# Performance work log

Measured on AMD Instinct MI355X. Metric: run time of the kernel, lower is better.

Reference implementation:

```python
import jax, jax.numpy as jnp
import numpy as np

EPS = 1e-5
L = 19        # number of semantic labels (fc_mu0..fc_mu18)
S = 512       # style_length


def conv3x3(x, w, b):
    # x: [B,C,H,W], w: [O,I,3,3] (torch OIHW), b: [O]
    y = jax.lax.conv_general_dilated(
        x, w, window_strides=(1, 1), padding='SAME',
        dimension_numbers=('NCHW', 'OIHW', 'NCHW'))
    return y + b[None, :, None, None]


def setup_inputs() -> dict:
    key = jax.random.key(0)
    ks = jax.random.split(key, 20)
    B, FIN, H, W = 4, 128, 256, 256
    inp = {
        'x': jax.random.normal(ks[0], (B, FIN, H, W), jnp.float32),
        'labels': jax.random.randint(ks[1], (B, H, W), 0, L),
        'noise': jax.random.normal(ks[2], (B, W, H, 1), jnp.float32),
        'style_codes': jax.random.normal(ks[3], (B, L, S), jnp.float32),
        # params
        'noise_var': 0.02 * jax.random.normal(ks[4], (FIN,), jnp.float32),
        'w_sh': 0.02 * jax.random.normal(ks[5], (128, L, 3, 3), jnp.float32),
        'b_sh': jnp.zeros((128,), jnp.float32),
        'w_g': 0.02 * jax.random.normal(ks[6], (FIN, 128, 3, 3), jnp.float32),
        'b_g': jnp.zeros((FIN,), jnp.float32),
        'w_b': 0.02 * jax.random.normal(ks[7], (FIN, 128, 3, 3), jnp.float32),
        'b_b': jnp.zeros((FIN,), jnp.float32),
        'Wfc': 0.02 * jax.random.normal(ks[8], (L, S, S), jnp.float32),  # [label, out, in]
        'bfc': jnp.zeros((L, S), jnp.float32),
        'w_cg': 0.02 * jax.random.normal(ks[9], (FIN, S, 3, 3), jnp.float32),
        'b_cg': jnp.zeros((FIN,), jnp.float32),
        'w_cb': 0.02 * jax.random.normal(ks[10], (FIN, S, 3, 3), jnp.float32),
        'b_cb': jnp.zeros((FIN,), jnp.float32),
        'g_blend': jnp.zeros((1,), jnp.float32),
        'b_blend': jnp.zeros((1,), jnp.float32),
    }
    return inp


def reference(x, labels, noise, style_codes, noise_var, w_sh, b_sh, w_g, b_g,
              w_b, b_b, Wfc, bfc, w_cg, b_cg, w_cb, b_cb, g_blend, b_blend):
    B, FIN, H, W = x.shape
    # added_noise: randn([B,W,H,1]) * noise_var[FIN] then transpose(1,3) -> [B,FIN,H,W]
    added = jnp.transpose(noise * noise_var, (0, 3, 2, 1))
    xn = x + added
    # param-free BatchNorm2d (training-mode batch stats, biased var)
    mean = jnp.mean(xn, axis=(0, 2, 3), keepdims=True)
    var = jnp.mean(jnp.square(xn - mean), axis=(0, 2, 3), keepdims=True)
    normalized = (xn - mean) / jnp.sqrt(var + EPS)

    # one-hot segmap [B,L,H,W]; interpolation to x's size is identity here
    seg = jnp.transpose(jax.nn.one_hot(labels, L, dtype=x.dtype), (0, 3, 1, 2))

    # per-label style FC: mu[b,j,:] = relu(fc_mu_j(style_codes[b,j]))
    mu = jax.nn.relu(jnp.einsum('bjd,jod->bjo', style_codes, Wfc) + bfc)  # [B,L,S]
    # masked_scatter with one-hot masks == per-pixel gather of the label's style code
    middle = mu[jnp.arange(B)[:, None, None], labels]        # [B,H,W,S]
    middle = jnp.transpose(middle, (0, 3, 1, 2))              # [B,S,H,W]

    gamma_avg = conv3x3(middle, w_cg, b_cg)
    beta_avg = conv3x3(middle, w_cb, b_cb)

    actv = jax.nn.relu(conv3x3(seg, w_sh, b_sh))
    gamma_spade = conv3x3(actv, w_g, b_g)
    beta_spade = conv3x3(actv, w_b, b_b)

    ga = jax.nn.sigmoid(g_blend)
    ba = jax.nn.sigmoid(b_blend)
    gamma_final = ga * gamma_avg + (1.0 - ga) * gamma_spade
    beta_final = ba * beta_avg + (1.0 - ba) * beta_spade
    return normalized * (1.0 + gamma_final) + beta_final
```

## Files before the change

kernel.cpp:

```cpp
#include <hip/hip_runtime.h>
#include <hip/hip_bf16.h>

#define NB   4
#define FIN  128
#define HH   256
#define WWW  256
#define LLAB 19
#define SSTY 512
#define HW   (HH*WWW)
#define NRED (NB*HW)

#define WS_NT   0
#define WS_SUM  262144
#define WS_SSQ  262272
#define WS_MEAN 262400
#define WS_ISTD 262528
#define WS_MU   262656
#define WS_A2   301568
#define WS_S1N  476672
#define WS_S2N  476673
#define WS_BSTG_B 1906752
#define WS_WSH_B  4855872

#define ASTRIDE 5200
#define OHSTRIDE 80

typedef __attribute__((ext_vector_type(8))) short bf16x8;
typedef __attribute__((ext_vector_type(4))) float f32x4;

__device__ inline unsigned short f2bf(float f) {
  __hip_bfloat16 h = __float2bfloat16(f);
  union { __hip_bfloat16 h; unsigned short u; } cv; cv.h = h; return cv.u;
}
__device__ inline float bf2f(short u) {
  union { unsigned int u; float f; } cv;
  cv.u = ((unsigned int)(unsigned short)u) << 16; return cv.f;
}

__device__ inline void gload_lds16(const void* g, void* l) {
  __builtin_amdgcn_global_load_lds(
      (const __attribute__((address_space(1))) void*)g,
      (__attribute__((address_space(3))) void*)l, 16, 0, 0);
}

__global__ __launch_bounds__(256) void kprep1(const float* __restrict__ noise,
                                              const float* __restrict__ style,
                                              const float* __restrict__ Wfc,
                                              const float* __restrict__ bfc,
                                              const float* __restrict__ w_g,
                                              const float* __restrict__ w_b,
                                              const float* __restrict__ w_sh,
                                              const float* __restrict__ g_blend,
                                              const float* __restrict__ b_blend,
                                              const float* __restrict__ x,
                                              char* __restrict__ wsb,
                                              float* __restrict__ ws) {
  const int t = threadIdx.x;
  if (blockIdx.x < 256) {
    __shared__ float tile[32][33];
    int blk = blockIdx.x;
    int b = blk >> 6, by = (blk >> 3) & 7, bx = blk & 7;
    int w0 = bx * 32, h0 = by * 32;
    int txx = t & 31, tyy = t >> 5;
    #pragma unroll
    for (int j = 0; j < 4; ++j) {
      int wi = w0 + tyy + j * 8;
      tile[tyy + j * 8][txx] = noise[(size_t)(b * 256 + wi) * 256 + h0 + txx];
    }
    __syncthreads();
    #pragma unroll
    for (int j = 0; j < 4; ++j) {
      int hi = h0 + tyy + j * 8;
      ws[WS_NT + (size_t)(b * 256 + hi) * 256 + w0 + txx] = tile[txx][tyy + j * 8];
    }
  } else if (blockIdx.x < 408) {
    int m = blockIdx.x - 256;
    int j = m >> 3, r = m & 7, b = r >> 1, half = r & 1;
    int o = half * 256 + t;
    const float4* wrow = (const float4*)(Wfc + ((size_t)j * 512 + o) * 512);
    const float4* srow = (const float4*)(style + ((size_t)b * 19 + j) * 512);
    float acc = 0.f;
    for (int d = 0; d < 128; ++d) {
      float4 w = wrow[d];
      float4 s = srow[d];
      acc = fmaf(w.x, s.x, acc); acc = fmaf(w.y, s.y, acc);
      acc = fmaf(w.z, s.z, acc); acc = fmaf(w.w, s.w, acc);
    }
    acc += bfc[j * 512 + o];
    ws[WS_MU + ((size_t)b * 19 + j) * 512 + o] = fmaxf(acc, 0.f);
  } else if (blockIdx.x < 552) {
    int tid = (blockIdx.x - 408) * 256 + t;
    int lane = tid & 63, grp = tid >> 6;
    int s36 = grp % 36, nb = grp / 36;
    int kk = s36 >> 2, cb = s36 & 3;
    int n = nb * 16 + (lane & 15);
    int conv = n & 1, cout = n >> 1;
    float blend = conv ? b_blend[0] : g_blend[0];
    float scale = 1.f - 1.f / (1.f + __expf(-blend));
    const float* src = conv ? w_b : w_g;
    bf16x8 v;
    #pragma unroll
    for (int i = 0; i < 8; ++i) {
      int k = s36 * 32 + (lane >> 4) * 8 + i;
      int kki = k >> 7, cin = k & 127;
      v[i] = (short)f2bf(scale * src[((size_t)cout * 128 + cin) * 9 + kki]);
    }
    size_t slot = (size_t)(kk * 5 + cb) * 16384 + (size_t)(nb * 64 + lane) * 16;
    #pragma unroll
    for (int bb2 = 0; bb2 < 4; ++bb2)
      *(bf16x8*)(wsb + WS_BSTG_B + (size_t)bb2 * 45 * 16384 + slot) = v;
  } else if (blockIdx.x < 642) {
    int tid = (blockIdx.x - 552) * 256 + t;
    if (tid < 23040) {
      int l = tid / 1152, r = tid % 1152, k = r >> 7, cin = r & 127;
      float v = (l == 0) ? 0.f : w_sh[((size_t)cin * 19 + (l - 1)) * 9 + k];
      ((unsigned short*)(wsb + WS_WSH_B))[tid] = f2bf(v);
    }
  } else if (blockIdx.x < 1154) {
    const int bc = blockIdx.x - 642;
    const int c = bc & 127;
    const float4* xp = (const float4*)(x + (size_t)bc * HW);
    float s1 = 0.f, s2 = 0.f;
    for (int i = 0; i < 64; ++i) {
      float4 xv = xp[i * 256 + t];
      s1 += xv.x + xv.y + xv.z + xv.w;
      s2 = fmaf(xv.x, xv.x, s2); s2 = fmaf(xv.y, xv.y, s2);
      s2 = fmaf(xv.z, xv.z, s2); s2 = fmaf(xv.w, xv.w, s2);
    }
    #pragma unroll
    for (int m = 32; m; m >>= 1) { s1 += __shfl_xor(s1, m); s2 += __shfl_xor(s2, m); }
    if ((t & 63) == 0) { atomicAdd(&ws[WS_SUM + c], s1); atomicAdd(&ws[WS_SSQ + c], s2); }
  } else {
    int blk = blockIdx.x - 1154;
    const float4* np = (const float4*)(noise + (size_t)blk * 16384);
    float s1 = 0.f, s2 = 0.f;
    for (int i = 0; i < 16; ++i) {
      float4 nz = np[i * 256 + t];
      s1 += nz.x + nz.y + nz.z + nz.w;
      s2 = fmaf(nz.x, nz.x, s2); s2 = fmaf(nz.y, nz.y, s2);
      s2 = fmaf(nz.z, nz.z, s2); s2 = fmaf(nz.w, nz.w, s2);
    }
    #pragma unroll
    for (int m = 32; m; m >>= 1) { s1 += __shfl_xor(s1, m); s2 += __shfl_xor(s2, m); }
    if ((t & 63) == 0) { atomicAdd(&ws[WS_S1N], s1); atomicAdd(&ws[WS_S2N], s2); }
  }
}

__global__ __launch_bounds__(512) void kprep2(const float* __restrict__ w_cg,
                                              const float* __restrict__ w_cb,
                                              float* __restrict__ ws) {
  const int t = threadIdx.x;
  __shared__ float wlds[32 * 288];
  const int blkm = blockIdx.x;
  const int cblk = blkm & 7, ssplit = (blkm >> 3) & 3, b = blkm >> 5;
  const int conv = t / 144, r = t % 144, cl = r / 9, k = r % 9;
  const int c = cblk * 16 + cl;
  const float* mu = ws + WS_MU;
  float acc[19];
  #pragma unroll
  for (int l = 0; l < 19; ++l) acc[l] = 0.f;

  for (int chunk = 0; chunk < 4; ++chunk) {
    const int s0 = ssplit * 128 + chunk * 32;
    for (int i = t; i < 9216; i += 512) {
      int kx = i % 9, q = i / 9, sl = q & 31, cc = q >> 5;
      int cv2 = cc >> 4, cl2 = cc & 15;
      const float* src = cv2 ? w_cb : w_cg;
      float v = src[((size_t)(cblk * 16 + cl2) * 512 + s0 + sl) * 9 + kx];
      wlds[sl * 288 + cv2 * 144 + cl2 * 9 + kx] = v;
    }
    __syncthreads();
    if (t < 288) {
      for (int sl = 0; sl < 32; ++sl) {
        float w = wlds[sl * 288 + t];
        int s = s0 + sl;
        #pragma unroll
        for (int l = 0; l < 19; ++l)
          acc[l] = fmaf(mu[((size_t)b * 19 + l) * 512 + s], w, acc[l]);
      }
    }
    __syncthreads();
  }
  if (t < 288) {
    #pragma unroll
    for (int l = 0; l < 19; ++l)
      atomicAdd(&ws[WS_A2 + (((size_t)b * 19 + l) * 9 + k) * 256 + conv * 128 + c], acc[l]);
  }
}

__global__ __launch_bounds__(256) void kprep3(const float* __restrict__ g_blend,
                                              const float* __restrict__ b_blend,
                                              const float* __restrict__ nvar,
                                              char* __restrict__ wsb,
                                              float* __restrict__ ws) {
  if (blockIdx.x == 0 && threadIdx.x < 128) {
    int c = threadIdx.x;
    float s1n = ws[WS_S1N], s2n = ws[WS_S2N];
    float nv = nvar[c];
    float mean = (ws[WS_SUM + c] + nv * s1n) / (float)NRED;
    float ex2 = (ws[WS_SSQ + c] + nv * nv * s2n) / (float)NRED;
    float var = ex2 - mean * mean;
    ws[WS_MEAN + c] = mean;
    ws[WS_ISTD + c] = 1.f / sqrtf(var + 1e-5f);
  }
  int tid = blockIdx.x * 256 + threadIdx.x;
  int lane = tid & 63, grp = tid >> 6;
  int kk = grp % 9, nb = (grp / 9) % 16, b = grp / 144;
  int n = nb * 16 + (lane & 15);
  int conv = n & 1, cout = n >> 1;
  float blend = conv ? b_blend[0] : g_blend[0];
  float scale = 1.f / (1.f + __expf(-blend));
  bf16x8 v;
  #pragma unroll
  for (int i = 0; i < 8; ++i) {
    int l = (lane >> 4) * 8 + i;
    float val = 0.f;
    if (l < 19)
      val = scale * ws[WS_A2 + (((size_t)b * 19 + l) * 9 + kk) * 256 + conv * 128 + cout];
    v[i] = (short)f2bf(val);
  }
  *(bf16x8*)(wsb + WS_BSTG_B + ((size_t)b * 45 + kk * 5 + 4) * 16384 +
             (size_t)(nb * 64 + lane) * 16) = v;
}

__global__ __launch_bounds__(1024, 4) void k_main(
    const float* __restrict__ x, const int* __restrict__ labels,
    const float* __restrict__ b_sh,
    const float* __restrict__ b_g, const float* __restrict__ b_b,
    const float* __restrict__ b_cg, const float* __restrict__ b_cb,
    const float* __restrict__ noise_var,
    const float* __restrict__ g_blend, const float* __restrict__ b_blend,
    const float* __restrict__ ws, float* __restrict__ out) {
  extern __shared__ char smem[];
  int* labt = (int*)smem;
  char* actv = smem + 1600;
  char* ohA  = smem + 84800;
  float* gbias = (float*)(smem + 110720);
  float* bbias = gbias + 128; float* nvl = gbias + 256;
  float* meanl = gbias + 384; float* istdl = gbias + 512; float* bshl = gbias + 640;
  char* bstg = smem + 113792;

  const int t = threadIdx.x;
  const int b = blockIdx.z;
  const int y0 = blockIdx.y * 16, x0 = blockIdx.x * 16;
  const char* wsb = (const char*)ws;
  const char* wshp = wsb + WS_WSH_B;

  if (t < 128) {
    float ga = 1.f / (1.f + __expf(-g_blend[0]));
    float ba = 1.f / (1.f + __expf(-b_blend[0]));
    gbias[t] = ga * b_cg[t] + (1.f - ga) * b_g[t];
    bbias[t] = ba * b_cb[t] + (1.f - ba) * b_b[t];
    nvl[t] = noise_var[t];
    meanl[t] = ws[WS_MEAN + t];
    istdl[t] = ws[WS_ISTD + t];
    bshl[t] = b_sh[t];
  }
  if (t < 400) {
    int ly = t / 20, lx = t % 20;
    int gy = y0 - 2 + ly, gx = x0 - 2 + lx;
    int v = 0;
    if ((unsigned)gy < 256u && (unsigned)gx < 256u)
      v = labels[((size_t)(b * 256 + gy)) * 256 + gx] + 1;
    labt[t] = v;
  }
  for (int i = t; i < 6480; i += 1024) ((unsigned int*)ohA)[i] = 0u;
  __syncthreads();

  for (int it = t; it < 5184; it += 1024) {
    int hp = it >> 4, cg = it & 15;
    int py = hp / 18, px = hp - py * 18;
    int gy = y0 - 1 + py, gx = x0 - 1 + px;
    int baddr = cg * ASTRIDE + hp * 16;
    bf16x8 o = {0, 0, 0, 0, 0, 0, 0, 0};
    if ((unsigned)gy < 256u && (unsigned)gx < 256u) {
      float accv[8];
      #pragma unroll
      for (int j = 0; j < 8; ++j) accv[j] = bshl[cg * 8 + j];
      #pragma unroll
      for (int k = 0; k < 9; ++k) {
        int dy = k / 3, dx = k - 3 * (k / 3);
        int lv = labt[(py + dy) * 20 + (px + dx)];
        bf16x8 wvv = *(const bf16x8*)(wshp + (size_t)((lv * 9 + k) * 128 + cg * 8) * 2);
        #pragma unroll
        for (int j = 0; j < 8; ++j) accv[j] += bf2f(wvv[j]);
      }
      #pragma unroll
      for (int j = 0; j < 8; ++j) o[j] = (short)f2bf(fmaxf(accv[j], 0.f));
    }
    *(bf16x8*)(actv + baddr) = o;
  }
  if (t < 324) {
    int py = t / 18, px = t - (t / 18) * 18;
    int gy = y0 - 1 + py, gx = x0 - 1 + px;
    if ((unsigned)gy < 256u && (unsigned)gx < 256u) {
      int lv = labt[(py + 1) * 20 + (px + 1)];
      ((unsigned short*)ohA)[t * 40 + (lv - 1)] = 0x3F80;
    }
  }
  __syncthreads();

  const int lane = t & 63;
  const int wid = t >> 6;
  const int wm = wid & 3, wn = wid >> 2;
  const int l15 = lane & 15, l16 = lane >> 4;

  const char* abase  = actv + l16 * ASTRIDE + (wm * 4 * 18 + l15) * 16;
  const char* ohbase = ohA + (wm * 4 * 18 + l15) * OHSTRIDE + l16 * 16;
  const char* bbase  = bstg + (wn * 4) * 1024 + lane * 16;
  const char* bsrc = wsb + WS_BSTG_B + (size_t)b * 45 * 16384 + (size_t)t * 16;
  char* ldsd0 = bstg + t * 16;
  char* ldsd1 = ldsd0 + 16384;
  char* ldsd2 = ldsd0 + 32768;

  f32x4 acc[4][4];
  #pragma unroll
  for (int i = 0; i < 4; ++i)
    #pragma unroll
    for (int j = 0; j < 4; ++j) acc[i][j] = (f32x4){0.f, 0.f, 0.f, 0.f};

#define PHASE(CB, KY, KX, RING, NXT, SOFF, DO_STAGE, VMC) { \
  asm volatile("s_waitcnt vmcnt(%0)" :: "i"(VMC) : "memory"); \
  __builtin_amdgcn_s_barrier(); \
  __builtin_amdgcn_sched_barrier(0); \
  if (DO_STAGE) gload_lds16(bsrc + (size_t)(SOFF) * 16384, NXT); \
  bf16x8 bfr_[4]; \
  _Pragma("unroll") \
  for (int nf_ = 0; nf_ < 4; ++nf_) \
    bfr_[nf_] = *(const bf16x8*)(bbase + (RING) * 16384 + nf_ * 1024); \
  bf16x8 af_[4]; \
  _Pragma("unroll") \
  for (int mf_ = 0; mf_ < 4; ++mf_) { \
    if ((CB) < 4) \
      af_[mf_] = *(const bf16x8*)(abase + (CB) * (4 * ASTRIDE) + ((mf_ + (KY)) * 18 + (KX)) * 16); \
    else \
      af_[mf_] = *(const bf16x8*)(ohbase + ((mf_ + (KY)) * 18 + (KX)) * OHSTRIDE); \
  } \
  __builtin_amdgcn_s_setprio(1); \
  _Pragma("unroll") \
  for (int mf_ = 0; mf_ < 4; ++mf_) \
    _Pragma("unroll") \
    for (int nf_ = 0; nf_ < 4; ++nf_) \
      acc[mf_][nf_] = __builtin_amdgcn_mfma_f32_16x16x32_bf16(af_[mf_], bfr_[nf_], acc[mf_][nf_], 0, 0, 0); \
  __builtin_amdgcn_s_setprio(0); }

  gload_lds16(bsrc, ldsd0);
  gload_lds16(bsrc + 16384, ldsd1);

  PHASE(0, 0, 0, 0, ldsd2,  2, true, 1)
  PHASE(1, 0, 0, 1, ldsd0,  3, true, 1)
  PHASE(2, 0, 0, 2, ldsd1,  4, true, 1)
  PHASE(3, 0, 0, 0, ldsd2,  5, true, 1)
  PHASE(4, 0, 0, 1, ldsd0,  6, true, 1)
  PHASE(0, 0, 1, 2, ldsd1,  7, true, 1)
  PHASE(1, 0, 1, 0, ldsd2,  8, true, 1)
  PHASE(2, 0, 1, 1, ldsd0,  9, true, 1)
  PHASE(3, 0, 1, 2, ldsd1, 10, true, 1)
  PHASE(4, 0, 1, 0, ldsd2, 11, true, 1)
  PHASE(0, 0, 2, 1, ldsd0, 12, true, 1)
  PHASE(1, 0, 2, 2, ldsd1, 13, true, 1)
  PHASE(2, 0, 2, 0, ldsd2, 14, true, 1)
  PHASE(3, 0, 2, 1, ldsd0, 15, true, 1)
  PHASE(4, 0, 2, 2, ldsd1, 16, true, 1)
  PHASE(0, 1, 0, 0, ldsd2, 17, true, 1)
  PHASE(1, 1, 0, 1, ldsd0, 18, true, 1)
  PHASE(2, 1, 0, 2, ldsd1, 19, true, 1)
  PHASE(3, 1, 0, 0, ldsd2, 20, true, 1)
  PHASE(4, 1, 0, 1, ldsd0, 21, true, 1)
  PHASE(0, 1, 1, 2, ldsd1, 22, true, 1)
  PHASE(1, 1, 1, 0, ldsd2, 23, true, 1)
  PHASE(2, 1, 1, 1, ldsd0, 24, true, 1)
  PHASE(3, 1, 1, 2, ldsd1, 25, true, 1)
  PHASE(4, 1, 1, 0, ldsd2, 26, true, 1)
  PHASE(0, 1, 2, 1, ldsd0, 27, true, 1)
  PHASE(1, 1, 2, 2, ldsd1, 28, true, 1)
  PHASE(2, 1, 2, 0, ldsd2, 29, true, 1)
  PHASE(3, 1, 2, 1, ldsd0, 30, true, 1)
  PHASE(4, 1, 2, 2, ldsd1, 31, true, 1)
  PHASE(0, 2, 0, 0, ldsd2, 32, true, 1)
  PHASE(1, 2, 0, 1, ldsd0, 33, true, 1)
  PHASE(2, 2, 0, 2, ldsd1, 34, true, 1)
  PHASE(3, 2, 0, 0, ldsd2, 35, true, 1)
  PHASE(4, 2, 0, 1, ldsd0, 36, true, 1)
  PHASE(0, 2, 1, 2, ldsd1, 37, true, 1)
  PHASE(1, 2, 1, 0, ldsd2, 38, true, 1)
  PHASE(2, 2, 1, 1, ldsd0, 39, true, 1)
  PHASE(3, 2, 1, 2, ldsd1, 40, true, 1)
  PHASE(4, 2, 1, 0, ldsd2, 41, true, 1)
  PHASE(0, 2, 2, 1, ldsd0, 42, true, 1)
  PHASE(1, 2, 2, 2, ldsd1, 43, true, 1)
  PHASE(2, 2, 2, 0, ldsd2, 44, true, 1)
  PHASE(3, 2, 2, 1, ldsd0,  0, false, 1)
  PHASE(4, 2, 2, 2, ldsd1,  0, false, 0)
#undef PHASE

  const float* nt = ws + WS_NT + (size_t)b * HW;
  float* eps = (float*)(smem + 1600);

  #pragma unroll
  for (int chunk = 0; chunk < 4; ++chunk) {
    __syncthreads();
    #pragma unroll
    for (int mf = 0; mf < 4; ++mf) {
      int widx = (wn * 16 + l15) * 260 + (wm * 4 + mf) * 16 + l16 * 4;
      *(f32x4*)(eps + widx) = acc[mf][chunk];
    }
    __syncthreads();
    #pragma unroll
    for (int rep = 0; rep < 2; ++rep) {
      int u = rep * 1024 + t;
      int xq = u & 3, y = (u >> 2) & 15, ci = u >> 6;
      int wnp = ci >> 3, qq = ci & 7;
      int c = wnp * 32 + chunk * 8 + qq;
      int rg = wnp * 16 + 2 * qq;
      f32x4 g4 = *(const f32x4*)(eps + rg * 260 + y * 16 + xq * 4);
      f32x4 b4 = *(const f32x4*)(eps + (rg + 1) * 260 + y * 16 + xq * 4);
      const float gb_ = gbias[c], bb_ = bbias[c];
      const float mn = meanl[c], is = istdl[c], nv = nvl[c];
      size_t off = (((size_t)(b * 128 + c)) * 256 + (y0 + y)) * 256 + x0 + xq * 4;
      float4 xv = *(const float4*)(x + off);
      float4 nz = *(const float4*)(nt + (y0 + y) * 256 + x0 + xq * 4);
      float4 o;
      o.x = ((xv.x + nv * nz.x) - mn) * is * (1.f + g4[0] + gb_) + (b4[0] + bb_);
      o.y = ((xv.y + nv * nz.y) - mn) * is * (1.f + g4[1] + gb_) + (b4[1] + bb_);
      o.z = ((xv.z + nv * nz.z) - mn) * is * (1.f + g4[2] + gb_) + (b4[2] + bb_);
      o.w = ((xv.w + nv * nz.w) - mn) * is * (1.f + g4[3] + gb_) + (b4[3] + bb_);
      *(float4*)(out + off) = o;
    }
  }
}

extern "C" void kernel_launch(void* const* d_in, const int* in_sizes, int n_in,
                              void* d_out, int out_size, void* d_ws, size_t ws_size,
                              hipStream_t stream) {
  const float* x        = (const float*)d_in[0];
  const int*   labels   = (const int*)d_in[1];
  const float* noise    = (const float*)d_in[2];
  const float* style    = (const float*)d_in[3];
  const float* nvar     = (const float*)d_in[4];
  const float* w_sh     = (const float*)d_in[5];
  const float* b_sh     = (const float*)d_in[6];
  const float* w_g      = (const float*)d_in[7];
  const float* b_g      = (const float*)d_in[8];
  const float* w_b      = (const float*)d_in[9];
  const float* b_b      = (const float*)d_in[10];
  const float* Wfc      = (const float*)d_in[11];
  const float* bfc      = (const float*)d_in[12];
  const float* w_cg     = (const float*)d_in[13];
  const float* b_cg     = (const float*)d_in[14];
  const float* w_cb     = (const float*)d_in[15];
  const float* b_cb     = (const float*)d_in[16];
  const float* g_blend  = (const float*)d_in[17];
  const float* b_blend  = (const float*)d_in[18];
  float* ws  = (float*)d_ws;
  char*  wsb = (char*)d_ws;
  float* out = (float*)d_out;

  static bool attr_set = false;
  if (!attr_set) {
    (void)hipFuncSetAttribute((const void*)k_main,
                              hipFuncAttributeMaxDynamicSharedMemorySize, 162944);
    attr_set = true;
  }

  hipMemsetAsync((char*)d_ws + (size_t)WS_SUM * 4, 0, 256 * 4, stream);
  hipMemsetAsync((char*)d_ws + (size_t)WS_A2 * 4, 0, (size_t)175106 * 4, stream);

  kprep1<<<dim3(1170), dim3(256), 0, stream>>>(noise, style, Wfc, bfc,
                                               w_g, w_b, w_sh, g_blend, b_blend,
                                               x, wsb, ws);
  kprep2<<<dim3(128), dim3(512), 0, stream>>>(w_cg, w_cb, ws);
  kprep3<<<dim3(144), dim3(256), 0, stream>>>(g_blend, b_blend, nvar, wsb, ws);
  k_main<<<dim3(16, 16, 4), dim3(1024), 162944, stream>>>(
      x, labels, b_sh, b_g, b_b, b_cg, b_cb,
      nvar, g_blend, b_blend, ws, out);
}
```

Baseline: 289.5 us.

## Switch main conv GEMM from bf16 to fp8 MFMA with scaled operands

```diff
diff --git a/kernel.cpp b/kernel.cpp
--- a/kernel.cpp
+++ b/kernel.cpp
@@ -20,10 +20,12 @@
 #define WS_S1N  476672
 #define WS_S2N  476673
 #define WS_BSTG_B 1906752
+#define BSTG_PER_B 368640
 #define WS_WSH_B  4855872
 
-#define ASTRIDE 5200
-#define OHSTRIDE 80
+#define ASTRIDE 2600
+#define OHSTRIDE 40
+#define ACCSCALE (1.f/256.f)
 
 typedef __attribute__((ext_vector_type(8))) short bf16x8;
 typedef __attribute__((ext_vector_type(4))) float f32x4;
@@ -35,6 +37,14 @@
 __device__ inline float bf2f(short u) {
   union { unsigned int u; float f; } cv;
   cv.u = ((unsigned int)(unsigned short)u) << 16; return cv.f;
+}
+
+__device__ inline long pack8_fp8(const float* v) {
+  int w0 = __builtin_amdgcn_cvt_pk_fp8_f32(v[0], v[1], 0, 0);
+  w0 = __builtin_amdgcn_cvt_pk_fp8_f32(v[2], v[3], w0, 1);
+  int w1 = __builtin_amdgcn_cvt_pk_fp8_f32(v[4], v[5], 0, 0);
+  w1 = __builtin_amdgcn_cvt_pk_fp8_f32(v[6], v[7], w1, 1);
+  return ((long)(unsigned)w1 << 32) | (unsigned)w0;
 }
 
 __device__ inline void gload_lds16(const void* g, void* l) {
@@ -96,19 +106,20 @@
     int n = nb * 16 + (lane & 15);
     int conv = n & 1, cout = n >> 1;
     float blend = conv ? b_blend[0] : g_blend[0];
-    float scale = 1.f - 1.f / (1.f + __expf(-blend));
+    float scale = 16.f * (1.f - 1.f / (1.f + __expf(-blend)));
     const float* src = conv ? w_b : w_g;
-    bf16x8 v;
+    float vv[8];
     #pragma unroll
     for (int i = 0; i < 8; ++i) {
       int k = s36 * 32 + (lane >> 4) * 8 + i;
       int kki = k >> 7, cin = k & 127;
-      v[i] = (short)f2bf(scale * src[((size_t)cout * 128 + cin) * 9 + kki]);
-    }
-    size_t slot = (size_t)(kk * 5 + cb) * 16384 + (size_t)(nb * 64 + lane) * 16;
+      vv[i] = scale * src[((size_t)cout * 128 + cin) * 9 + kki];
+    }
+    long pv = pack8_fp8(vv);
+    size_t slot = (size_t)(kk * 5 + cb) * 8192 + (size_t)(nb * 64 + lane) * 8;
     #pragma unroll
     for (int bb2 = 0; bb2 < 4; ++bb2)
-      *(bf16x8*)(wsb + WS_BSTG_B + (size_t)bb2 * 45 * 16384 + slot) = v;
+      *(long*)(wsb + WS_BSTG_B + (size_t)bb2 * BSTG_PER_B + slot) = pv;
   } else if (blockIdx.x < 642) {
     int tid = (blockIdx.x - 552) * 256 + t;
     if (tid < 23040) {
@@ -209,18 +220,19 @@
   int n = nb * 16 + (lane & 15);
   int conv = n & 1, cout = n >> 1;
   float blend = conv ? b_blend[0] : g_blend[0];
-  float scale = 1.f / (1.f + __expf(-blend));
-  bf16x8 v;
+  float scale = 16.f / (1.f + __expf(-blend));
+  float vv[8];
   #pragma unroll
   for (int i = 0; i < 8; ++i) {
     int l = (lane >> 4) * 8 + i;
     float val = 0.f;
     if (l < 19)
       val = scale * ws[WS_A2 + (((size_t)b * 19 + l) * 9 + kk) * 256 + conv * 128 + cout];
-    v[i] = (short)f2bf(val);
-  }
-  *(bf16x8*)(wsb + WS_BSTG_B + ((size_t)b * 45 + kk * 5 + 4) * 16384 +
-             (size_t)(nb * 64 + lane) * 16) = v;
+    vv[i] = val;
+  }
+  long pv = pack8_fp8(vv);
+  *(long*)(wsb + WS_BSTG_B + (size_t)b * BSTG_PER_B +
+           (size_t)(kk * 5 + 4) * 8192 + (size_t)(nb * 64 + lane) * 8) = pv;
 }
 
 __global__ __launch_bounds__(1024, 4) void k_main(
@@ -234,17 +246,18 @@
   extern __shared__ char smem[];
   int* labt = (int*)smem;
   char* actv = smem + 1600;
-  char* ohA  = smem + 84800;
-  float* gbias = (float*)(smem + 110720);
+  char* ohA  = smem + 43200;
+  float* gbias = (float*)(smem + 68160);
   float* bbias = gbias + 128; float* nvl = gbias + 256;
   float* meanl = gbias + 384; float* istdl = gbias + 512; float* bshl = gbias + 640;
-  char* bstg = smem + 113792;
+  char* bstg = smem + 71232;
 
   const int t = threadIdx.x;
   const int b = blockIdx.z;
   const int y0 = blockIdx.y * 16, x0 = blockIdx.x * 16;
   const char* wsb = (const char*)ws;
   const char* wshp = wsb + WS_WSH_B;
+  const bool stg = (t < 512);
 
   if (t < 128) {
     float ga = 1.f / (1.f + __expf(-g_blend[0]));
@@ -264,15 +277,15 @@
       v = labels[((size_t)(b * 256 + gy)) * 256 + gx] + 1;
     labt[t] = v;
   }
-  for (int i = t; i < 6480; i += 1024) ((unsigned int*)ohA)[i] = 0u;
+  for (int i = t; i < 3240; i += 1024) ((unsigned int*)ohA)[i] = 0u;
   __syncthreads();
 
   for (int it = t; it < 5184; it += 1024) {
     int hp = it >> 4, cg = it & 15;
     int py = hp / 18, px = hp - py * 18;
     int gy = y0 - 1 + py, gx = x0 - 1 + px;
-    int baddr = cg * ASTRIDE + hp * 16;
-    bf16x8 o = {0, 0, 0, 0, 0, 0, 0, 0};
+    int baddr = cg * ASTRIDE + hp * 8;
+    long o = 0;
     if ((unsigned)gy < 256u && (unsigned)gx < 256u) {
       float accv[8];
       #pragma unroll
@@ -286,16 +299,17 @@
         for (int j = 0; j < 8; ++j) accv[j] += bf2f(wvv[j]);
       }
       #pragma unroll
-      for (int j = 0; j < 8; ++j) o[j] = (short)f2bf(fmaxf(accv[j], 0.f));
-    }
-    *(bf16x8*)(actv + baddr) = o;
+      for (int j = 0; j < 8; ++j) accv[j] = fmaxf(accv[j], 0.f) * 16.f;
+      o = pack8_fp8(accv);
+    }
+    *(long*)(actv + baddr) = o;
   }
   if (t < 324) {
     int py = t / 18, px = t - (t / 18) * 18;
     int gy = y0 - 1 + py, gx = x0 - 1 + px;
     if ((unsigned)gy < 256u && (unsigned)gx < 256u) {
       int lv = labt[(py + 1) * 20 + (px + 1)];
-      ((unsigned short*)ohA)[t * 40 + (lv - 1)] = 0x3F80;
+      ((unsigned char*)ohA)[t * OHSTRIDE + (lv - 1)] = 0x58;
     }
   }
   __syncthreads();
@@ -305,13 +319,13 @@
   const int wm = wid & 3, wn = wid >> 2;
   const int l15 = lane & 15, l16 = lane >> 4;
 
-  const char* abase  = actv + l16 * ASTRIDE + (wm * 4 * 18 + l15) * 16;
-  const char* ohbase = ohA + (wm * 4 * 18 + l15) * OHSTRIDE + l16 * 16;
-  const char* bbase  = bstg + (wn * 4) * 1024 + lane * 16;
-  const char* bsrc = wsb + WS_BSTG_B + (size_t)b * 45 * 16384 + (size_t)t * 16;
+  const char* abase  = actv + l16 * ASTRIDE + (wm * 4 * 18 + l15) * 8;
+  const char* ohbase = ohA + (wm * 4 * 18 + l15) * OHSTRIDE + l16 * 8;
+  const char* bbase  = bstg + (wn * 4) * 512 + lane * 8;
+  const char* bsrc = wsb + WS_BSTG_B + (size_t)b * BSTG_PER_B + (size_t)t * 16;
   char* ldsd0 = bstg + t * 16;
-  char* ldsd1 = ldsd0 + 16384;
-  char* ldsd2 = ldsd0 + 32768;
+  char* ldsd1 = ldsd0 + 8192;
+  char* ldsd2 = ldsd0 + 16384;
 
   f32x4 acc[4][4];
   #pragma unroll
@@ -323,29 +337,31 @@
   asm volatile("s_waitcnt vmcnt(%0)" :: "i"(VMC) : "memory"); \
   __builtin_amdgcn_s_barrier(); \
   __builtin_amdgcn_sched_barrier(0); \
-  if (DO_STAGE) gload_lds16(bsrc + (size_t)(SOFF) * 16384, NXT); \
-  bf16x8 bfr_[4]; \
+  if ((DO_STAGE) && stg) gload_lds16(bsrc + (size_t)(SOFF) * 8192, NXT); \
+  long bfr_[4]; \
   _Pragma("unroll") \
   for (int nf_ = 0; nf_ < 4; ++nf_) \
-    bfr_[nf_] = *(const bf16x8*)(bbase + (RING) * 16384 + nf_ * 1024); \
-  bf16x8 af_[4]; \
+    bfr_[nf_] = *(const long*)(bbase + (RING) * 8192 + nf_ * 512); \
+  long af_[4]; \
   _Pragma("unroll") \
   for (int mf_ = 0; mf_ < 4; ++mf_) { \
     if ((CB) < 4) \
-      af_[mf_] = *(const bf16x8*)(abase + (CB) * (4 * ASTRIDE) + ((mf_ + (KY)) * 18 + (KX)) * 16); \
+      af_[mf_] = *(const long*)(abase + (CB) * (4 * ASTRIDE) + ((mf_ + (KY)) * 18 + (KX)) * 8); \
     else \
-      af_[mf_] = *(const bf16x8*)(ohbase + ((mf_ + (KY)) * 18 + (KX)) * OHSTRIDE); \
+      af_[mf_] = *(const long*)(ohbase + ((mf_ + (KY)) * 18 + (KX)) * OHSTRIDE); \
   } \
   __builtin_amdgcn_s_setprio(1); \
   _Pragma("unroll") \
   for (int mf_ = 0; mf_ < 4; ++mf_) \
     _Pragma("unroll") \
     for (int nf_ = 0; nf_ < 4; ++nf_) \
-      acc[mf_][nf_] = __builtin_amdgcn_mfma_f32_16x16x32_bf16(af_[mf_], bfr_[nf_], acc[mf_][nf_], 0, 0, 0); \
+      acc[mf_][nf_] = __builtin_amdgcn_mfma_f32_16x16x32_fp8_fp8(af_[mf_], bfr_[nf_], acc[mf_][nf_], 0, 0, 0); \
   __builtin_amdgcn_s_setprio(0); }
 
-  gload_lds16(bsrc, ldsd0);
-  gload_lds16(bsrc + 16384, ldsd1);
+  if (stg) {
+    gload_lds16(bsrc, ldsd0);
+    gload_lds16(bsrc + 8192, ldsd1);
+  }
 
   PHASE(0, 0, 0, 0, ldsd2,  2, true, 1)
   PHASE(1, 0, 0, 1, ldsd0,  3, true, 1)
@@ -403,7 +419,7 @@
     #pragma unroll
     for (int mf = 0; mf < 4; ++mf) {
       int widx = (wn * 16 + l15) * 260 + (wm * 4 + mf) * 16 + l16 * 4;
-      *(f32x4*)(eps + widx) = acc[mf][chunk];
+      *(f32x4*)(eps + widx) = acc[mf][chunk] * ACCSCALE;
     }
     __syncthreads();
     #pragma unroll
@@ -459,7 +475,7 @@
   static bool attr_set = false;
   if (!attr_set) {
     (void)hipFuncSetAttribute((const void*)k_main,
-                              hipFuncAttributeMaxDynamicSharedMemorySize, 162944);
+                              hipFuncAttributeMaxDynamicSharedMemorySize, 95808);
     attr_set = true;
   }
 
@@ -471,7 +487,7 @@
                                                x, wsb, ws);
   kprep2<<<dim3(128), dim3(512), 0, stream>>>(w_cg, w_cb, ws);
   kprep3<<<dim3(144), dim3(256), 0, stream>>>(g_blend, b_blend, nvar, wsb, ws);
-  k_main<<<dim3(16, 16, 4), dim3(1024), 162944, stream>>>(
+  k_main<<<dim3(16, 16, 4), dim3(1024), 95808, stream>>>(
       x, labels, b_sh, b_g, b_b, b_cg, b_cb,
       nvar, g_blend, b_blend, ws, out);
 }
```

Result: no change. 289.0 us (-0.2%).
